# Performance work log

Hardware: AMD Instinct MI355X
Metric: run time of the kernel (lower is better)

The kernel has to match this reference:

```python
import jax, jax.numpy as jnp
import numpy as np

D_MODEL = 1024
D_K = 1024
D_V = 1024
N_HEAD = 16
EPS = 1e-5
BS, N_TOK = 2, 2048


def setup_inputs() -> dict:
    key = jax.random.key(0)
    ks = jax.random.split(key, 12)
    s = 0.02
    q = jax.random.normal(ks[0], (BS, N_TOK, D_MODEL), jnp.float32)
    k = jax.random.normal(ks[1], (BS, N_TOK, D_MODEL), jnp.float32)
    v = jax.random.normal(ks[2], (BS, N_TOK, D_MODEL), jnp.float32)
    return {
        "q": q, "k": k, "v": v,
        "gamma": jnp.ones((D_MODEL,), jnp.float32),
        "beta": jnp.zeros((D_MODEL,), jnp.float32),
        "Wq": jax.random.normal(ks[3], (D_MODEL, D_K), jnp.float32) * s,
        "bq": jnp.zeros((D_K,), jnp.float32),
        "Wk": jax.random.normal(ks[4], (D_MODEL, D_K), jnp.float32) * s,
        "bk": jnp.zeros((D_K,), jnp.float32),
        "Wv": jax.random.normal(ks[5], (D_MODEL, D_V), jnp.float32) * s,
        "bv": jnp.zeros((D_V,), jnp.float32),
        "Wo": jax.random.normal(ks[6], (D_V, D_MODEL), jnp.float32) * s,
        "bo": jnp.zeros((D_MODEL,), jnp.float32),
    }


def reference(q, k, v, gamma, beta, Wq, bq, Wk, bk, Wv, bv, Wo, bo):
    # NOTE: original module ignores k, v args; self-attention over q.
    bs, n_tok, d_m = q.shape
    d_h = D_K // N_HEAD
    temper = float(np.sqrt(d_h))

    # LayerNorm1d over d_model
    mu = jnp.mean(q, axis=-1, keepdims=True)
    var = jnp.var(q, axis=-1, keepdims=True)
    h = (q - mu) / jnp.sqrt(var + EPS) * gamma + beta

    # projections; head split = chunk along feature dim -> [bs, H, T, d_h]
    qh = (h @ Wq + bq).reshape(bs, n_tok, N_HEAD, d_h).transpose(0, 2, 1, 3)
    kh = (h @ Wk + bk).reshape(bs, n_tok, N_HEAD, d_h).transpose(0, 2, 1, 3)
    vh = jax.nn.relu(h @ Wv + bv).reshape(bs, n_tok, N_HEAD, d_h).transpose(0, 2, 1, 3)

    scores = jnp.einsum('bhqd,bhkd->bhqk', qh, kh) / temper
    # dropout before softmax in train mode; identity in eval (deterministic ref)
    attn = jax.nn.softmax(scores, axis=-1)
    o = jnp.einsum('bhqk,bhkd->bhqd', attn, vh)  # [bs, H, T, d_h]

    # faithful to torch: view(bs, n_tok, -1) with NO head transpose (head-major merge)
    merged = o.reshape(bs, n_tok, N_HEAD * d_h)
    out = merged @ Wo + bo + q  # proj + residual
    return out
```

## Files before the change

kernel.cpp:

```cpp
#include <hip/hip_runtime.h>

typedef __bf16 bf16;
typedef __bf16 bf16x8 __attribute__((ext_vector_type(8)));
typedef __bf16 bf16x4 __attribute__((ext_vector_type(4)));
typedef float  f32x4  __attribute__((ext_vector_type(4)));
typedef float  f32x16 __attribute__((ext_vector_type(16)));
typedef unsigned int u32;
typedef u32 u32x4 __attribute__((ext_vector_type(4)));

#define AS1U(p) ((const __attribute__((address_space(1))) unsigned int*)(p))
#define AS3U(p) ((__attribute__((address_space(3))) unsigned int*)(p))

static __device__ __forceinline__ u32 pack2(float a, float b) {
    unsigned short ua = __builtin_bit_cast(unsigned short, (bf16)a);
    unsigned short ub = __builtin_bit_cast(unsigned short, (bf16)b);
    return (u32)ua | ((u32)ub << 16);
}

template <int VM>
static __device__ __forceinline__ void wait_vm() {
    if constexpr (VM == 8)      asm volatile("s_waitcnt vmcnt(8)" ::: "memory");
    else if constexpr (VM == 4) asm volatile("s_waitcnt vmcnt(4)" ::: "memory");
    else                        asm volatile("s_waitcnt vmcnt(0)" ::: "memory");
}

__global__ void transpose_cast4_kernel(const float* __restrict__ W0, const float* __restrict__ W1,
                                       const float* __restrict__ W2, const float* __restrict__ W3,
                                       bf16* __restrict__ D0, bf16* __restrict__ D1,
                                       bf16* __restrict__ D2, bf16* __restrict__ D3) {
    __shared__ float tile[32][33];
    const float* W; bf16* D;
    switch (blockIdx.z) {
        case 0: W = W0; D = D0; break;
        case 1: W = W1; D = D1; break;
        case 2: W = W2; D = D2; break;
        default: W = W3; D = D3; break;
    }
    const int bj = blockIdx.x, bi = blockIdx.y;
    const int tx = threadIdx.x, ty = threadIdx.y;
#pragma unroll
    for (int i = 0; i < 4; i++) {
        tile[ty + i * 8][tx] = W[(size_t)(bi * 32 + ty + i * 8) * 1024 + bj * 32 + tx];
    }
    __syncthreads();
#pragma unroll
    for (int i = 0; i < 4; i++) {
        D[(size_t)(bj * 32 + ty + i * 8) * 1024 + bi * 32 + tx] =
            (bf16)tile[tx][ty + i * 8];
    }
}

__global__ void layernorm_kernel(const float* __restrict__ x,
                                 const float* __restrict__ gamma,
                                 const float* __restrict__ beta,
                                 bf16* __restrict__ h) {
    const int row = blockIdx.x;
    const float* xr = x + (size_t)row * 1024;
    const int t = threadIdx.x;
    float4 v = ((const float4*)xr)[t];
    float s  = v.x + v.y + v.z + v.w;
    float s2 = v.x * v.x + v.y * v.y + v.z * v.z + v.w * v.w;
#pragma unroll
    for (int m = 1; m < 64; m <<= 1) {
        s  += __shfl_xor(s, m, 64);
        s2 += __shfl_xor(s2, m, 64);
    }
    __shared__ float ssum[4], ssum2[4];
    const int wid = t >> 6, lane = t & 63;
    if (lane == 0) { ssum[wid] = s; ssum2[wid] = s2; }
    __syncthreads();
    s  = ssum[0] + ssum[1] + ssum[2] + ssum[3];
    s2 = ssum2[0] + ssum2[1] + ssum2[2] + ssum2[3];
    const float mu  = s * (1.f / 1024.f);
    const float var = s2 * (1.f / 1024.f) - mu * mu;
    const float rs  = rsqrtf(var + 1e-5f);
    float4 g = ((const float4*)gamma)[t];
    float4 b = ((const float4*)beta)[t];
    bf16x4 o;
    o[0] = (bf16)((v.x - mu) * rs * g.x + b.x);
    o[1] = (bf16)((v.y - mu) * rs * g.y + b.y);
    o[2] = (bf16)((v.z - mu) * rs * g.z + b.z);
    o[3] = (bf16)((v.w - mu) * rs * g.w + b.w);
    ((bf16x4*)(h + (size_t)row * 1024))[t] = o;
}

template <int EPI>
__global__ void gemm_kernel(const bf16* __restrict__ A, const bf16* __restrict__ BT,
                            int N, int K,
                            bf16* __restrict__ Cb,
                            const float* __restrict__ b0, const float* __restrict__ b1,
                            const float* __restrict__ b2, bf16* __restrict__ Vt,
                            float* __restrict__ Cf, const float* __restrict__ bo,
                            const float* __restrict__ resid) {
    __shared__ bf16 Asm[128][32];
    __shared__ bf16 Bsm[128][32];
    const int tid = threadIdx.x;
    const int lane = tid & 63, wave = tid >> 6;
    const int wr = wave >> 1, wc = wave & 1;
    const int tileN = blockIdx.x * 128, tileM = blockIdx.y * 128;
    const int row16 = lane & 15, g = lane >> 4;

    f32x4 acc[4][4] = {};

    for (int kt = 0; kt < K; kt += 32) {
#pragma unroll
        for (int i = 0; i < 2; i++) {
            int c = tid + i * 256;
            int r = c >> 2, cb = (c & 3) * 16;
            const char* g_ = (const char*)(A + (size_t)(tileM + r) * K + kt) + cb;
            char* l_ = (char*)&Asm[0][0] + c * 16;
            __builtin_amdgcn_global_load_lds(AS1U(g_), AS3U(l_), 16, 0, 0);
        }
#pragma unroll
        for (int i = 0; i < 2; i++) {
            int c = tid + i * 256;
            int r = c >> 2, cb = (c & 3) * 16;
            const char* g_ = (const char*)(BT + (size_t)(tileN + r) * K + kt) + cb;
            char* l_ = (char*)&Bsm[0][0] + c * 16;
            __builtin_amdgcn_global_load_lds(AS1U(g_), AS3U(l_), 16, 0, 0);
        }
        __syncthreads();
        bf16x8 af[4], bfr[4];
#pragma unroll
        for (int m = 0; m < 4; m++)
            af[m] = *(const bf16x8*)&Asm[wr * 64 + m * 16 + row16][g * 8];
#pragma unroll
        for (int n = 0; n < 4; n++)
            bfr[n] = *(const bf16x8*)&Bsm[wc * 64 + n * 16 + row16][g * 8];
#pragma unroll
        for (int m = 0; m < 4; m++)
#pragma unroll
            for (int n = 0; n < 4; n++)
                acc[m][n] = __builtin_amdgcn_mfma_f32_16x16x32_bf16(af[m], bfr[n],
                                                                   acc[m][n], 0, 0, 0);
        __syncthreads();
    }
#pragma unroll
    for (int m = 0; m < 4; m++) {
        const int row = tileM + wr * 64 + m * 16 + g * 4;
#pragma unroll
        for (int n = 0; n < 4; n++) {
            const int col = tileN + wc * 64 + n * 16 + row16;
            if (EPI == 0 && col >= 2048) {
                const int d = col - 2048;
                const float bias = b2[d];
                bf16x4 pk;
#pragma unroll
                for (int j = 0; j < 4; j++) {
                    float v = acc[m][n][j] + bias;
                    pk[j] = (bf16)fmaxf(v, 0.f);
                }
                const int bb = row >> 11, tt = row & 2047;
                const int hh = d >> 6, dd = d & 63;
                *(bf16x4*)&Vt[(((size_t)bb * 16 + hh) * 64 + dd) * 2048 + tt] = pk;
            } else {
#pragma unroll
                for (int j = 0; j < 4; j++) {
                    float v = acc[m][n][j];
                    const int r = row + j;
                    if (EPI == 0) {
                        if (col < 1024) {
                            v = (v + b0[col]) * 0.18033688011112042f;
                        } else {
                            v += b1[col - 1024];
                        }
                        Cb[(size_t)r * N + col] = (bf16)v;
                    } else {
                        v += bo[col] + resid[(size_t)r * N + col];
                        Cf[(size_t)r * N + col] = v;
                    }
                }
            }
        }
    }
}

__global__ __launch_bounds__(256, 2)
void attn_kernel(const bf16* __restrict__ qkv, const bf16* __restrict__ Vt,
                 bf16* __restrict__ Obuf) {
    const int bid = blockIdx.x;
    const int swz = (bid & 7) * 64 + (bid >> 3);
    const int bh = swz >> 4, qt = swz & 15;
    const int b = bh >> 4, h = bh & 15;
    const int qbase = qt * 128;
    const int tid = threadIdx.x;
    const int lane = tid & 63, wv = tid >> 6;
    const int c = lane & 31, p = lane >> 5;

    __shared__ bf16 Kl[4][64][64];
    __shared__ bf16 Vl[4][64][64];

    const bf16* qrow = qkv + (size_t)(b * 2048 + qbase + wv * 32 + c) * 3072 + h * 64;
    bf16x8 qf[4];
#pragma unroll
    for (int ch = 0; ch < 4; ch++)
        qf[ch] = *(const bf16x8*)(qrow + ch * 16 + p * 8);

    const char* kgbase = (const char*)(qkv + (size_t)b * 2048 * 3072 + 1024 + h * 64);
    const char* vgbase = (const char*)(Vt + (size_t)bh * 64 * 2048);
    int kgo[2], vgo[2];
#pragma unroll
    for (int i = 0; i < 2; i++) {
        const int cc = tid + i * 256;
        const int srow = cc >> 3;
        const int scol = ((cc & 7) * 16) ^ ((srow & 7) << 4);
        kgo[i] = srow * 6144 + scol;
        vgo[i] = srow * 4096 + scol;
    }

    auto stage = [&](int t, int slot) {
        const size_t ko = (size_t)t * 64 * 6144;
        const size_t vo = (size_t)t * 128;
        char* kb = (char*)&Kl[slot][0][0];
        char* vb = (char*)&Vl[slot][0][0];
#pragma unroll
        for (int i = 0; i < 2; i++) {
            const int cc16 = (tid + i * 256) * 16;
            __builtin_amdgcn_global_load_lds(AS1U(kgbase + ko + kgo[i]), AS3U(kb + cc16), 16, 0, 0);
            __builtin_amdgcn_global_load_lds(AS1U(vgbase + vo + vgo[i]), AS3U(vb + cc16), 16, 0, 0);
        }
    };

    f32x16 accO[2] = {};
    float l_r = 0.f;

    auto compute = [&](int slot) {
        const char* Kb = (const char*)&Kl[slot][0][0];
        const char* Vb = (const char*)&Vl[slot][0][0];
#pragma unroll
        for (int cc = 0; cc < 2; cc++) {
            f32x16 accT = {};
            const int tok = cc * 32 + c;
#pragma unroll
            for (int ch = 0; ch < 4; ch++) {
                const bf16x8 kf = *(const bf16x8*)(Kb + tok * 128 +
                                                   ((ch * 32 + p * 16) ^ ((tok & 7) << 4)));
                accT = __builtin_amdgcn_mfma_f32_32x32x16_bf16(kf, qf[ch], accT, 0, 0, 0);
            }
            float pv[16];
            float s = 0.f;
#pragma unroll
            for (int r = 0; r < 16; r++) {
                pv[r] = exp2f(accT[r]);
                s += pv[r];
            }
            l_r += s;
            u32 k01 = pack2(pv[0], pv[1]),  k23 = pack2(pv[2], pv[3]);
            u32 k45 = pack2(pv[4], pv[5]),  k67 = pack2(pv[6], pv[7]);
            u32 k89 = pack2(pv[8], pv[9]),  kab = pack2(pv[10], pv[11]);
            u32 kcd = pack2(pv[12], pv[13]), kef = pack2(pv[14], pv[15]);
            asm("v_permlane32_swap_b32 %0, %1" : "+v"(k45), "+v"(k01));
            asm("v_permlane32_swap_b32 %0, %1" : "+v"(k67), "+v"(k23));
            asm("v_permlane32_swap_b32 %0, %1" : "+v"(kcd), "+v"(k89));
            asm("v_permlane32_swap_b32 %0, %1" : "+v"(kef), "+v"(kab));
            u32x4 w0w = {k01, k23, k45, k67};
            u32x4 w1w = {k89, kab, kcd, kef};
            const bf16x8 pf0 = __builtin_bit_cast(bf16x8, w0w);
            const bf16x8 pf1 = __builtin_bit_cast(bf16x8, w1w);
#pragma unroll
            for (int dc = 0; dc < 2; dc++) {
                const int rd = dc * 32 + c;
                const int sw = (rd & 7) << 4;
                const bf16x8 vf0 = *(const bf16x8*)(Vb + rd * 128 + ((cc * 64 + p * 16) ^ sw));
                const bf16x8 vf1 = *(const bf16x8*)(Vb + rd * 128 + ((cc * 64 + 32 + p * 16) ^ sw));
                accO[dc] = __builtin_amdgcn_mfma_f32_32x32x16_bf16(pf0, vf0, accO[dc], 0, 0, 0);
                accO[dc] = __builtin_amdgcn_mfma_f32_32x32x16_bf16(pf1, vf1, accO[dc], 0, 0, 0);
            }
        }
    };

    stage(0, 0);
    stage(1, 1);
    stage(2, 2);

    for (int t = 0; t < 29; ++t) {
        wait_vm<8>();
        __builtin_amdgcn_s_barrier();
        asm volatile("" ::: "memory");
        stage(t + 3, (t + 3) & 3);
        compute(t & 3);
    }
    wait_vm<8>(); __builtin_amdgcn_s_barrier(); asm volatile("" ::: "memory");
    compute(29 & 3);
    wait_vm<4>(); __builtin_amdgcn_s_barrier(); asm volatile("" ::: "memory");
    compute(30 & 3);
    wait_vm<0>(); __builtin_amdgcn_s_barrier(); asm volatile("" ::: "memory");
    compute(31 & 3);

    l_r += __shfl_xor(l_r, 32);
    const float linv = 1.f / l_r;
    float li[16];
#pragma unroll
    for (int r = 0; r < 16; r++)
        li[r] = __shfl(linv, (r & 3) + 8 * (r >> 2) + 4 * p);
    bf16* ob = Obuf + ((size_t)bh * 2048 + qbase + wv * 32) * 64;
#pragma unroll
    for (int dc = 0; dc < 2; dc++)
#pragma unroll
        for (int r = 0; r < 16; r++) {
            const int row = (r & 3) + 8 * (r >> 2) + 4 * p;
            ob[(size_t)row * 64 + dc * 32 + c] = (bf16)(accO[dc][r] * li[r]);
        }
}

extern "C" void kernel_launch(void* const* d_in, const int* in_sizes, int n_in,
                              void* d_out, int out_size, void* d_ws, size_t ws_size,
                              hipStream_t stream) {
    const float* q     = (const float*)d_in[0];
    const float* gamma = (const float*)d_in[3];
    const float* beta  = (const float*)d_in[4];
    const float* Wq    = (const float*)d_in[5];
    const float* bq    = (const float*)d_in[6];
    const float* Wk    = (const float*)d_in[7];
    const float* bk    = (const float*)d_in[8];
    const float* Wv    = (const float*)d_in[9];
    const float* bv    = (const float*)d_in[10];
    const float* Wo    = (const float*)d_in[11];
    const float* bo    = (const float*)d_in[12];
    float* out = (float*)d_out;

    char* ws = (char*)d_ws;
    bf16* h     = (bf16*)(ws);
    bf16* WcatT = (bf16*)(ws + (8u << 20));
    bf16* WoT   = (bf16*)(ws + (14u << 20));
    bf16* qkv   = (bf16*)(ws + (16u << 20));
    bf16* Obuf  = (bf16*)(ws + (40u << 20));
    bf16* Vtb   = (bf16*)(ws + (48u << 20));

    transpose_cast4_kernel<<<dim3(32, 32, 4), dim3(32, 8), 0, stream>>>(
        Wq, Wk, Wv, Wo,
        WcatT, WcatT + (size_t)1024 * 1024, WcatT + (size_t)2048 * 1024, WoT);

    layernorm_kernel<<<4096, 256, 0, stream>>>(q, gamma, beta, h);

    gemm_kernel<0><<<dim3(24, 32), 256, 0, stream>>>(h, WcatT, 3072, 1024,
                                                     qkv, bq, bk, bv, Vtb,
                                                     nullptr, nullptr, nullptr);

    attn_kernel<<<512, 256, 0, stream>>>(qkv, Vtb, Obuf);

    gemm_kernel<1><<<dim3(8, 32), 256, 0, stream>>>(Obuf, WoT, 1024, 1024,
                                                    nullptr, nullptr, nullptr, nullptr, nullptr,
                                                    out, bo, q);
}
```

Measured before the change: 147.8 us.

## Split attention KV range across two wave groups and merge partial sums

The attention kernel now launches 512 threads per block. Two groups of four waves each process half of the key/value sequence, each with its own double-buffered LDS tiles. The partial output accumulators and row sums are then combined through shared memory before normalisation. The aim is more waves in flight and shorter per-wave serial loops, at the cost of a shallower prefetch pipeline (double instead of quad buffering with full vmcnt(0) waits), an extra LDS reduction step, and register pressure under the new launch bounds. The softmax sum is also rewritten as a tree reduction.

```diff
diff --git a/kernel.cpp b/kernel.cpp
--- a/kernel.cpp
+++ b/kernel.cpp
@@ -15,13 +15,6 @@
     unsigned short ua = __builtin_bit_cast(unsigned short, (bf16)a);
     unsigned short ub = __builtin_bit_cast(unsigned short, (bf16)b);
     return (u32)ua | ((u32)ub << 16);
-}
-
-template <int VM>
-static __device__ __forceinline__ void wait_vm() {
-    if constexpr (VM == 8)      asm volatile("s_waitcnt vmcnt(8)" ::: "memory");
-    else if constexpr (VM == 4) asm volatile("s_waitcnt vmcnt(4)" ::: "memory");
-    else                        asm volatile("s_waitcnt vmcnt(0)" ::: "memory");
 }
 
 __global__ void transpose_cast4_kernel(const float* __restrict__ W0, const float* __restrict__ W1,
@@ -175,7 +168,7 @@
     }
 }
 
-__global__ __launch_bounds__(256, 2)
+__global__ __launch_bounds__(512, 4)
 void attn_kernel(const bf16* __restrict__ qkv, const bf16* __restrict__ Vt,
                  bf16* __restrict__ Obuf) {
     const int bid = blockIdx.x;
@@ -185,39 +178,43 @@
     const int qbase = qt * 128;
     const int tid = threadIdx.x;
     const int lane = tid & 63, wv = tid >> 6;
+    const int half = wv >> 2, qw = wv & 3;
     const int c = lane & 31, p = lane >> 5;
 
-    __shared__ bf16 Kl[4][64][64];
-    __shared__ bf16 Vl[4][64][64];
-
-    const bf16* qrow = qkv + (size_t)(b * 2048 + qbase + wv * 32 + c) * 3072 + h * 64;
+    __shared__ bf16 Kl[2][2][64][64];
+    __shared__ bf16 Vl[2][2][64][64];
+
+    const bf16* qrow = qkv + (size_t)(b * 2048 + qbase + qw * 32 + c) * 3072 + h * 64;
     bf16x8 qf[4];
 #pragma unroll
     for (int ch = 0; ch < 4; ch++)
         qf[ch] = *(const bf16x8*)(qrow + ch * 16 + p * 8);
 
-    const char* kgbase = (const char*)(qkv + (size_t)b * 2048 * 3072 + 1024 + h * 64);
-    const char* vgbase = (const char*)(Vt + (size_t)bh * 64 * 2048);
-    int kgo[2], vgo[2];
+    const char* kgbase = (const char*)(qkv + (size_t)b * 2048 * 3072 + 1024 + h * 64)
+                         + (size_t)(half * 1024) * 6144;
+    const char* vgbase = (const char*)(Vt + (size_t)bh * 64 * 2048) + half * 2048;
+    const int ht = tid & 255;
+    const char* kgp[2]; const char* vgp[2]; int ldo[2];
 #pragma unroll
     for (int i = 0; i < 2; i++) {
-        const int cc = tid + i * 256;
+        const int cc = ht + i * 256;
         const int srow = cc >> 3;
         const int scol = ((cc & 7) * 16) ^ ((srow & 7) << 4);
-        kgo[i] = srow * 6144 + scol;
-        vgo[i] = srow * 4096 + scol;
-    }
+        kgp[i] = kgbase + (size_t)srow * 6144 + scol;
+        vgp[i] = vgbase + (size_t)srow * 4096 + scol;
+        ldo[i] = cc * 16;
+    }
+    char* kldb = (char*)&Kl[half][0][0][0];
+    char* vldb = (char*)&Vl[half][0][0][0];
 
     auto stage = [&](int t, int slot) {
-        const size_t ko = (size_t)t * 64 * 6144;
+        const size_t ko = (size_t)t * (64 * 6144);
         const size_t vo = (size_t)t * 128;
-        char* kb = (char*)&Kl[slot][0][0];
-        char* vb = (char*)&Vl[slot][0][0];
+        const int sb = slot * 8192;
 #pragma unroll
         for (int i = 0; i < 2; i++) {
-            const int cc16 = (tid + i * 256) * 16;
-            __builtin_amdgcn_global_load_lds(AS1U(kgbase + ko + kgo[i]), AS3U(kb + cc16), 16, 0, 0);
-            __builtin_amdgcn_global_load_lds(AS1U(vgbase + vo + vgo[i]), AS3U(vb + cc16), 16, 0, 0);
+            __builtin_amdgcn_global_load_lds(AS1U(kgp[i] + ko), AS3U(kldb + sb + ldo[i]), 16, 0, 0);
+            __builtin_amdgcn_global_load_lds(AS1U(vgp[i] + vo), AS3U(vldb + sb + ldo[i]), 16, 0, 0);
         }
     };
 
@@ -225,8 +222,8 @@
     float l_r = 0.f;
 
     auto compute = [&](int slot) {
-        const char* Kb = (const char*)&Kl[slot][0][0];
-        const char* Vb = (const char*)&Vl[slot][0][0];
+        const char* Kb = (const char*)&Kl[half][slot][0][0];
+        const char* Vb = (const char*)&Vl[half][slot][0][0];
 #pragma unroll
         for (int cc = 0; cc < 2; cc++) {
             f32x16 accT = {};
@@ -238,13 +235,13 @@
                 accT = __builtin_amdgcn_mfma_f32_32x32x16_bf16(kf, qf[ch], accT, 0, 0, 0);
             }
             float pv[16];
-            float s = 0.f;
-#pragma unroll
-            for (int r = 0; r < 16; r++) {
-                pv[r] = exp2f(accT[r]);
-                s += pv[r];
-            }
-            l_r += s;
+#pragma unroll
+            for (int r = 0; r < 16; r++) pv[r] = exp2f(accT[r]);
+            float s01 = (pv[0] + pv[1]) + (pv[2] + pv[3]);
+            float s23 = (pv[4] + pv[5]) + (pv[6] + pv[7]);
+            float s45 = (pv[8] + pv[9]) + (pv[10] + pv[11]);
+            float s67 = (pv[12] + pv[13]) + (pv[14] + pv[15]);
+            l_r += (s01 + s23) + (s45 + s67);
             u32 k01 = pack2(pv[0], pv[1]),  k23 = pack2(pv[2], pv[3]);
             u32 k45 = pack2(pv[4], pv[5]),  k67 = pack2(pv[6], pv[7]);
             u32 k89 = pack2(pv[8], pv[9]),  kab = pack2(pv[10], pv[11]);
@@ -269,38 +266,54 @@
         }
     };
 
+#define KV_SYNC() do { \
+        asm volatile("s_waitcnt vmcnt(0)" ::: "memory"); \
+        __builtin_amdgcn_s_barrier(); \
+        asm volatile("" ::: "memory"); \
+    } while (0)
+
     stage(0, 0);
-    stage(1, 1);
-    stage(2, 2);
-
-    for (int t = 0; t < 29; ++t) {
-        wait_vm<8>();
-        __builtin_amdgcn_s_barrier();
-        asm volatile("" ::: "memory");
-        stage(t + 3, (t + 3) & 3);
-        compute(t & 3);
-    }
-    wait_vm<8>(); __builtin_amdgcn_s_barrier(); asm volatile("" ::: "memory");
-    compute(29 & 3);
-    wait_vm<4>(); __builtin_amdgcn_s_barrier(); asm volatile("" ::: "memory");
-    compute(30 & 3);
-    wait_vm<0>(); __builtin_amdgcn_s_barrier(); asm volatile("" ::: "memory");
-    compute(31 & 3);
-
-    l_r += __shfl_xor(l_r, 32);
-    const float linv = 1.f / l_r;
-    float li[16];
-#pragma unroll
-    for (int r = 0; r < 16; r++)
-        li[r] = __shfl(linv, (r & 3) + 8 * (r >> 2) + 4 * p);
-    bf16* ob = Obuf + ((size_t)bh * 2048 + qbase + wv * 32) * 64;
-#pragma unroll
-    for (int dc = 0; dc < 2; dc++)
-#pragma unroll
-        for (int r = 0; r < 16; r++) {
-            const int row = (r & 3) + 8 * (r >> 2) + 4 * p;
-            ob[(size_t)row * 64 + dc * 32 + c] = (bf16)(accO[dc][r] * li[r]);
-        }
+#pragma unroll 1
+    for (int t = 0; t < 14; t += 2) {
+        KV_SYNC(); stage(t + 1, 1); compute(0);
+        KV_SYNC(); stage(t + 2, 0); compute(1);
+    }
+    KV_SYNC(); stage(15, 1); compute(0);
+    KV_SYNC(); compute(1);
+#undef KV_SYNC
+
+    __syncthreads();
+    float* ex = (float*)&Kl[0][0][0][0];
+    const int xb = (qw * 64 + lane) * 33;
+    if (half) {
+#pragma unroll
+        for (int dc = 0; dc < 2; dc++)
+#pragma unroll
+            for (int r = 0; r < 16; r++) ex[xb + dc * 16 + r] = accO[dc][r];
+        ex[xb + 32] = l_r;
+    }
+    __syncthreads();
+    if (!half) {
+#pragma unroll
+        for (int dc = 0; dc < 2; dc++)
+#pragma unroll
+            for (int r = 0; r < 16; r++) accO[dc][r] += ex[xb + dc * 16 + r];
+        l_r += ex[xb + 32];
+        l_r += __shfl_xor(l_r, 32);
+        const float linv = 1.f / l_r;
+        float li[16];
+#pragma unroll
+        for (int r = 0; r < 16; r++)
+            li[r] = __shfl(linv, (r & 3) + 8 * (r >> 2) + 4 * p);
+        bf16* ob = Obuf + ((size_t)bh * 2048 + qbase + qw * 32) * 64;
+#pragma unroll
+        for (int dc = 0; dc < 2; dc++)
+#pragma unroll
+            for (int r = 0; r < 16; r++) {
+                const int row = (r & 3) + 8 * (r >> 2) + 4 * p;
+                ob[(size_t)row * 64 + dc * 32 + c] = (bf16)(accO[dc][r] * li[r]);
+            }
+    }
 }
 
 extern "C" void kernel_launch(void* const* d_in, const int* in_sizes, int n_in,
@@ -337,7 +350,7 @@
                                                      qkv, bq, bk, bv, Vtb,
                                                      nullptr, nullptr, nullptr);
 
-    attn_kernel<<<512, 256, 0, stream>>>(qkv, Vtb, Obuf);
+    attn_kernel<<<512, 512, 0, stream>>>(qkv, Vtb, Obuf);
 
     gemm_kernel<1><<<dim3(8, 32), 256, 0, stream>>>(Obuf, WoT, 1024, 1024,
                                                     nullptr, nullptr, nullptr, nullptr, nullptr,
```

Measured after the change: 143.5 us. 1.03x faster.
